# Optimization experiments

Measured on AMD Instinct MI355X. Metric: run time of the kernel, lower is better.

## Reference

```python
import jax, jax.numpy as jnp
import numpy as np

B, N, D, H, O = 20000, 32, 128, 256, 128
ATT_SLOPE = 0.01   # nn.LeakyReLU() default inside self.att
ALPHA = 0.2        # leakyrelu slope for attention scores


def _lrelu(v, slope):
    return jnp.where(v > 0, v, slope * v)


def setup_inputs() -> dict:
    key = jax.random.key(0)
    ks = jax.random.split(key, 6)
    x = jax.random.normal(ks[0], (B, D), dtype=jnp.float32)
    neibs = jax.random.normal(ks[1], (B * N, D), dtype=jnp.float32)
    # torch Linear weight is [out,in]; we store transposed [in,out] for x @ W
    W_att = jax.random.normal(ks[2], (D, H), dtype=jnp.float32) / np.sqrt(D)
    W_fcx = jax.random.normal(ks[3], (D, O), dtype=jnp.float32) / np.sqrt(D)
    W_fcn = jax.random.normal(ks[4], (D, O), dtype=jnp.float32) / np.sqrt(D)
    a = jax.random.normal(ks[5], (2 * H, 1), dtype=jnp.float32) * (1.414 * np.sqrt(6.0 / (2 * H + 1)))
    return {"x": x, "neibs": neibs, "W_att": W_att, "W_fcx": W_fcx, "W_fcn": W_fcn, "a": a}


def reference(x, neibs, W_att, W_fcx, W_fcn, a):
    b = x.shape[0]
    n = neibs.shape[0] // b
    # self.att = Linear(no bias) + LeakyReLU(default 0.01)
    x_att = _lrelu(x @ W_att, ATT_SLOPE)                       # [B,H]
    neib_att = _lrelu(neibs @ W_att, ATT_SLOPE).reshape(b, n, -1)  # [B,N,H]
    # cat([x_att.repeat, neib_att]) @ a  ==  x_att @ a[:H] + neib_att @ a[H:]
    h = W_att.shape[1]
    e = _lrelu(x_att @ a[:h, 0] + neib_att @ a[h:, 0][..., None] if False else
               (x_att @ a[:h, 0])[:, None] + jnp.einsum('bnh,h->bn', neib_att, a[h:, 0]), ALPHA)  # [B,N]
    attention = jax.nn.softmax(e, axis=1)                      # softmax over neighbors
    # dropout skipped (eval mode / training=False)
    agg_neib = jnp.einsum('bnd,bn->bd', neibs.reshape(b, n, -1), attention)  # [B,D]
    out = jnp.concatenate([x @ W_fcx, agg_neib @ W_fcn], axis=1)  # combine_fn = cat dim=1
    out = jax.nn.relu(out)                                     # activation
    return out
```

## Files before the change

### kernel.cpp

```cpp
#include <hip/hip_runtime.h>
#include <hip/hip_bf16.h>


#define BB 20000
#define NN 32
#define DD 128
#define HH 256
#define OO 128
#define MB 4
#define ROWS 144
#define AG0 132

typedef __bf16 bf16x8 __attribute__((ext_vector_type(8)));
typedef __bf16 bf16x4 __attribute__((ext_vector_type(4)));
typedef float f32x4 __attribute__((ext_vector_type(4)));

__global__ void prep_weights(const float* __restrict__ Watt,
                             const float* __restrict__ Wfcx,
                             const float* __restrict__ Wfcn,
                             __bf16* __restrict__ WaT,
                             __bf16* __restrict__ WcT) {
    int idx = blockIdx.x * 256 + threadIdx.x;
    int half = idx >> 15;
    int j = idx & 32767;
    int c = j >> 7, k = j & 127;
    if (half == 0) {
        WaT[j] = (__bf16)Watt[k * HH + c];
    } else {
        float wv = (c < OO) ? Wfcx[k * OO + c] : Wfcn[k * OO + (c - OO)];
        WcT[j] = (__bf16)wv;
    }
}

__launch_bounds__(256, 4)
__global__ void gat_fused(const float* __restrict__ x,
                          const float* __restrict__ neibs,
                          const float* __restrict__ a,
                          const __bf16* __restrict__ WaT,
                          const __bf16* __restrict__ WcT,
                          float* __restrict__ out) {
    __shared__ __bf16 rowsS[ROWS * 128];
    __shared__ float e_part[4][ROWS];
    __shared__ float att_s[MB][NN];

    const int tid = threadIdx.x;
    const int w   = tid >> 6;
    const int l   = tid & 63;
    const int lr  = l & 15;
    const int lg  = l >> 4;
    const int b0  = blockIdx.x * MB;
    char* rbase = (char*)rowsS;

    const int stbase = (tid >> 5) * 256 + ((8 * (tid & 31)) ^ ((tid >> 5) << 4));
    int abase[4];
#pragma unroll
    for (int ks = 0; ks < 4; ++ks)
        abase[ks] = lr * 256 + ((ks * 64 + lg * 16) ^ ((lr & 7) << 4));

    {
        const float4* np4 = (const float4*)(neibs + (size_t)b0 * NN * DD);
#pragma unroll
        for (int it = 0; it < 16; ++it) {
            float4 v = np4[it * 256 + tid];
            bf16x4 s = { (__bf16)v.x, (__bf16)v.y, (__bf16)v.z, (__bf16)v.w };
            *(bf16x4*)(rbase + stbase + it * 2048) = s;
        }
        if (tid < 128) {
            float4 v = ((const float4*)(x + (size_t)b0 * DD))[tid];
            bf16x4 s = { (__bf16)v.x, (__bf16)v.y, (__bf16)v.z, (__bf16)v.w };
            *(bf16x4*)(rbase + stbase + 32768) = s;
        }
    }

    bf16x8 bw[4][4];
    float cN[4][4];
#pragma unroll
    for (int c4 = 0; c4 < 4; ++c4) {
        int col = (w * 4 + c4) * 16 + lr;
#pragma unroll
        for (int ks = 0; ks < 4; ++ks)
            bw[c4][ks] = *(const bf16x8*)(WaT + col * 128 + ks * 32 + lg * 8);
#pragma unroll
        for (int i = 0; i < 4; ++i)
            cN[c4][i] = a[HH + (w * 4 + c4) * 16 + 4 * lg + i];
    }

    __syncthreads();

#pragma unroll
    for (int rt = 0; rt < 8; ++rt) {
        bf16x8 af[4];
#pragma unroll
        for (int ks = 0; ks < 4; ++ks)
            af[ks] = *(const bf16x8*)(rbase + abase[ks] + rt * 4096);
        f32x4 acc[4];
#pragma unroll
        for (int c4 = 0; c4 < 4; ++c4) acc[c4] = (f32x4){0.f, 0.f, 0.f, 0.f};
#pragma unroll
        for (int ks = 0; ks < 4; ++ks)
#pragma unroll
            for (int c4 = 0; c4 < 4; ++c4)
                acc[c4] = __builtin_amdgcn_mfma_f32_16x16x32_bf16(bw[c4][ks], af[ks], acc[c4], 0, 0, 0);
        float ep = 0.f;
#pragma unroll
        for (int c4 = 0; c4 < 4; ++c4)
#pragma unroll
            for (int i = 0; i < 4; ++i) {
                float v = acc[c4][i];
                ep = fmaf(cN[c4][i], fmaxf(v, 0.01f * v), ep);
            }
        ep += __shfl_xor(ep, 16);
        ep += __shfl_xor(ep, 32);
        if (l < 16) e_part[w][rt * 16 + l] = ep;
    }
    {
#pragma unroll
        for (int c4 = 0; c4 < 4; ++c4)
#pragma unroll
            for (int i = 0; i < 4; ++i)
                cN[c4][i] = a[(w * 4 + c4) * 16 + 4 * lg + i];
        bf16x8 af[4];
#pragma unroll
        for (int ks = 0; ks < 4; ++ks)
            af[ks] = *(const bf16x8*)(rbase + abase[ks] + 32768);
        f32x4 acc[4];
#pragma unroll
        for (int c4 = 0; c4 < 4; ++c4) acc[c4] = (f32x4){0.f, 0.f, 0.f, 0.f};
#pragma unroll
        for (int ks = 0; ks < 4; ++ks)
#pragma unroll
            for (int c4 = 0; c4 < 4; ++c4)
                acc[c4] = __builtin_amdgcn_mfma_f32_16x16x32_bf16(bw[c4][ks], af[ks], acc[c4], 0, 0, 0);
        float ep = 0.f;
#pragma unroll
        for (int c4 = 0; c4 < 4; ++c4)
#pragma unroll
            for (int i = 0; i < 4; ++i) {
                float v = acc[c4][i];
                ep = fmaf(cN[c4][i], fmaxf(v, 0.01f * v), ep);
            }
        ep += __shfl_xor(ep, 16);
        ep += __shfl_xor(ep, 32);
        if (l < 16) e_part[w][128 + l] = ep;
    }
    __syncthreads();

    if (tid < 128) {
        const int bloc = tid >> 5;
        const int nloc = tid & 31;
        float sn = e_part[0][tid] + e_part[1][tid] + e_part[2][tid] + e_part[3][tid];
        float sx = e_part[0][128 + bloc] + e_part[1][128 + bloc] +
                   e_part[2][128 + bloc] + e_part[3][128 + bloc];
        float e = sx + sn;
        e = (e > 0.f) ? e : 0.2f * e;
        float mx = e;
#pragma unroll
        for (int m = 16; m >= 1; m >>= 1) mx = fmaxf(mx, __shfl_xor(mx, m, 32));
        float ex = __expf(e - mx);
        float sum = ex;
#pragma unroll
        for (int m = 16; m >= 1; m >>= 1) sum += __shfl_xor(sum, m, 32);
        att_s[bloc][nloc] = ex / sum;
    }
    __syncthreads();

    bf16x8 bff[4][4];
#pragma unroll
    for (int c4 = 0; c4 < 4; ++c4)
#pragma unroll
        for (int ks = 0; ks < 4; ++ks)
            bff[c4][ks] = *(const bf16x8*)(WcT + ((w * 4 + c4) * 16 + lr) * 128 + ks * 32 + lg * 8);

    {
        const int half = l >> 5, li = l & 31;
        const int agbase = w * 8192 + 256 * half + ((8 * li) ^ (half << 4));
        float ag[4] = {0.f, 0.f, 0.f, 0.f};
#pragma unroll
        for (int i = 0; i < 16; ++i) {
            float wv = att_s[w][2 * i + half];
            bf16x4 v = *(const bf16x4*)(rbase + (agbase ^ ((2 * i & 7) << 4)) + 512 * i);
#pragma unroll
            for (int j = 0; j < 4; ++j) ag[j] = fmaf(wv, (float)v[j], ag[j]);
        }
#pragma unroll
        for (int j = 0; j < 4; ++j) ag[j] += __shfl_xor(ag[j], 32);
        if (half == 0) {
            int row = AG0 + w;
            int off = row * 256 + ((8 * li) ^ ((row & 7) << 4));
            bf16x4 s = { (__bf16)ag[0], (__bf16)ag[1], (__bf16)ag[2], (__bf16)ag[3] };
            *(bf16x4*)(rbase + off) = s;
        }
    }
    __syncthreads();

    {
        bf16x8 af[4];
#pragma unroll
        for (int ks = 0; ks < 4; ++ks)
            af[ks] = *(const bf16x8*)(rbase + abase[ks] + 32768);
        f32x4 acc[4];
#pragma unroll
        for (int c4 = 0; c4 < 4; ++c4) acc[c4] = (f32x4){0.f, 0.f, 0.f, 0.f};
#pragma unroll
        for (int ks = 0; ks < 4; ++ks)
#pragma unroll
            for (int c4 = 0; c4 < 4; ++c4)
                acc[c4] = __builtin_amdgcn_mfma_f32_16x16x32_bf16(af[ks], bff[c4][ks], acc[c4], 0, 0, 0);
#pragma unroll
        for (int c4 = 0; c4 < 4; ++c4) {
            int col = (w * 4 + c4) * 16 + lr;
#pragma unroll
            for (int reg = 0; reg < 4; ++reg) {
                int i = lg * 4 + reg;
                bool doit = (col < 128) ? (i < 4) : (i >= 4 && i < 8);
                if (doit) {
                    float v = fmaxf(acc[c4][reg], 0.f);
                    out[(size_t)(b0 + (i & 3)) * 256 + col] = v;
                }
            }
        }
    }
}

extern "C" void kernel_launch(void* const* d_in, const int* in_sizes, int n_in,
                              void* d_out, int out_size, void* d_ws, size_t ws_size,
                              hipStream_t stream) {
    const float* x    = (const float*)d_in[0];
    const float* nb   = (const float*)d_in[1];
    const float* Watt = (const float*)d_in[2];
    const float* Wfcx = (const float*)d_in[3];
    const float* Wfcn = (const float*)d_in[4];
    const float* a    = (const float*)d_in[5];
    __bf16* WaT = (__bf16*)d_ws;
    __bf16* WcT = WaT + 32768;
    float* o = (float*)d_out;

    prep_weights<<<256, 256, 0, stream>>>(Watt, Wfcx, Wfcn, WaT, WcT);
    gat_fused<<<BB / MB, 256, 0, stream>>>(x, nb, a, WaT, WcT, o);
}
```

Measured before the change: 126.6 us.

## Load MFMA operands directly from global memory instead of staging rows in LDS

Removes the 36KB LDS staging buffer for neighbor and x rows. Each wave now loads fp32 operands straight from global memory and converts them to bf16 in registers for the attention MFMAs. The softmax result stays in registers and is broadcast by shuffle, so the att_s array and one barrier go away. The aggregation re-reads neighbor rows from global memory (likely L2 hits) in fp32 instead of bf16 from LDS. The much smaller LDS footprint should allow higher occupancy, at the cost of more global and L2 traffic with less coalesced per-lane access.

```diff
diff --git a/kernel.cpp b/kernel.cpp
--- a/kernel.cpp
+++ b/kernel.cpp
@@ -8,12 +8,15 @@
 #define HH 256
 #define OO 128
 #define MB 4
-#define ROWS 144
-#define AG0 132
 
 typedef __bf16 bf16x8 __attribute__((ext_vector_type(8)));
-typedef __bf16 bf16x4 __attribute__((ext_vector_type(4)));
+typedef __bf16 bf16x2 __attribute__((ext_vector_type(2)));
 typedef float f32x4 __attribute__((ext_vector_type(4)));
+
+__device__ __forceinline__ bf16x8 cvt8(float4 u, float4 v) {
+    return (bf16x8){ (__bf16)u.x, (__bf16)u.y, (__bf16)u.z, (__bf16)u.w,
+                     (__bf16)v.x, (__bf16)v.y, (__bf16)v.z, (__bf16)v.w };
+}
 
 __global__ void prep_weights(const float* __restrict__ Watt,
                              const float* __restrict__ Wfcx,
@@ -39,9 +42,8 @@
                           const __bf16* __restrict__ WaT,
                           const __bf16* __restrict__ WcT,
                           float* __restrict__ out) {
-    __shared__ __bf16 rowsS[ROWS * 128];
-    __shared__ float e_part[4][ROWS];
-    __shared__ float att_s[MB][NN];
+    __shared__ float e_part[4][144];
+    __shared__ __bf16 aggL[4 * 136];
 
     const int tid = threadIdx.x;
     const int w   = tid >> 6;
@@ -49,28 +51,7 @@
     const int lr  = l & 15;
     const int lg  = l >> 4;
     const int b0  = blockIdx.x * MB;
-    char* rbase = (char*)rowsS;
-
-    const int stbase = (tid >> 5) * 256 + ((8 * (tid & 31)) ^ ((tid >> 5) << 4));
-    int abase[4];
-#pragma unroll
-    for (int ks = 0; ks < 4; ++ks)
-        abase[ks] = lr * 256 + ((ks * 64 + lg * 16) ^ ((lr & 7) << 4));
-
-    {
-        const float4* np4 = (const float4*)(neibs + (size_t)b0 * NN * DD);
-#pragma unroll
-        for (int it = 0; it < 16; ++it) {
-            float4 v = np4[it * 256 + tid];
-            bf16x4 s = { (__bf16)v.x, (__bf16)v.y, (__bf16)v.z, (__bf16)v.w };
-            *(bf16x4*)(rbase + stbase + it * 2048) = s;
-        }
-        if (tid < 128) {
-            float4 v = ((const float4*)(x + (size_t)b0 * DD))[tid];
-            bf16x4 s = { (__bf16)v.x, (__bf16)v.y, (__bf16)v.z, (__bf16)v.w };
-            *(bf16x4*)(rbase + stbase + 32768) = s;
-        }
-    }
+    const float* nb = neibs + (size_t)b0 * NN * DD;
 
     bf16x8 bw[4][4];
     float cN[4][4];
@@ -85,14 +66,14 @@
             cN[c4][i] = a[HH + (w * 4 + c4) * 16 + 4 * lg + i];
     }
 
-    __syncthreads();
-
 #pragma unroll
     for (int rt = 0; rt < 8; ++rt) {
         bf16x8 af[4];
 #pragma unroll
-        for (int ks = 0; ks < 4; ++ks)
-            af[ks] = *(const bf16x8*)(rbase + abase[ks] + rt * 4096);
+        for (int ks = 0; ks < 4; ++ks) {
+            const float* p = nb + (rt * 16 + lr) * 128 + ks * 32 + lg * 8;
+            af[ks] = cvt8(*(const float4*)p, *(const float4*)(p + 4));
+        }
         f32x4 acc[4];
 #pragma unroll
         for (int c4 = 0; c4 < 4; ++c4) acc[c4] = (f32x4){0.f, 0.f, 0.f, 0.f};
@@ -119,10 +100,13 @@
 #pragma unroll
             for (int i = 0; i < 4; ++i)
                 cN[c4][i] = a[(w * 4 + c4) * 16 + 4 * lg + i];
+        const float* xp = x + (size_t)(b0 + (lr & 3)) * 128;
         bf16x8 af[4];
 #pragma unroll
-        for (int ks = 0; ks < 4; ++ks)
-            af[ks] = *(const bf16x8*)(rbase + abase[ks] + 32768);
+        for (int ks = 0; ks < 4; ++ks) {
+            const float* p = xp + ks * 32 + lg * 8;
+            af[ks] = cvt8(*(const float4*)p, *(const float4*)(p + 4));
+        }
         f32x4 acc[4];
 #pragma unroll
         for (int c4 = 0; c4 < 4; ++c4) acc[c4] = (f32x4){0.f, 0.f, 0.f, 0.f};
@@ -145,13 +129,13 @@
     }
     __syncthreads();
 
-    if (tid < 128) {
-        const int bloc = tid >> 5;
-        const int nloc = tid & 31;
-        float sn = e_part[0][tid] + e_part[1][tid] + e_part[2][tid] + e_part[3][tid];
-        float sx = e_part[0][128 + bloc] + e_part[1][128 + bloc] +
-                   e_part[2][128 + bloc] + e_part[3][128 + bloc];
-        float e = sx + sn;
+    float att;
+    {
+        const int nl = l & 31;
+        const int idx = w * 32 + nl;
+        const int xr = 128 + w;
+        float e = e_part[0][idx] + e_part[1][idx] + e_part[2][idx] + e_part[3][idx]
+                + e_part[0][xr]  + e_part[1][xr]  + e_part[2][xr]  + e_part[3][xr];
         e = (e > 0.f) ? e : 0.2f * e;
         float mx = e;
 #pragma unroll
@@ -160,44 +144,46 @@
         float sum = ex;
 #pragma unroll
         for (int m = 16; m >= 1; m >>= 1) sum += __shfl_xor(sum, m, 32);
-        att_s[bloc][nloc] = ex / sum;
+        att = ex / sum;
+    }
+
+    bf16x8 bff[4][4];
+#pragma unroll
+    for (int c4 = 0; c4 < 4; ++c4)
+#pragma unroll
+        for (int ks = 0; ks < 4; ++ks)
+            bff[c4][ks] = *(const bf16x8*)(WcT + ((w * 4 + c4) * 16 + lr) * 128 + ks * 32 + lg * 8);
+
+    {
+        const float* rp = nb + (w * 32) * 128 + 2 * l;
+        float ag0 = 0.f, ag1 = 0.f;
+#pragma unroll 8
+        for (int n = 0; n < 32; ++n) {
+            float wv = __shfl(att, n);
+            float2 v = *(const float2*)(rp + n * 128);
+            ag0 = fmaf(wv, v.x, ag0);
+            ag1 = fmaf(wv, v.y, ag1);
+        }
+        bf16x2 s = { (__bf16)ag0, (__bf16)ag1 };
+        *(bf16x2*)((char*)aggL + w * 272 + 4 * l) = s;
     }
     __syncthreads();
 
-    bf16x8 bff[4][4];
-#pragma unroll
-    for (int c4 = 0; c4 < 4; ++c4)
-#pragma unroll
-        for (int ks = 0; ks < 4; ++ks)
-            bff[c4][ks] = *(const bf16x8*)(WcT + ((w * 4 + c4) * 16 + lr) * 128 + ks * 32 + lg * 8);
-
-    {
-        const int half = l >> 5, li = l & 31;
-        const int agbase = w * 8192 + 256 * half + ((8 * li) ^ (half << 4));
-        float ag[4] = {0.f, 0.f, 0.f, 0.f};
-#pragma unroll
-        for (int i = 0; i < 16; ++i) {
-            float wv = att_s[w][2 * i + half];
-            bf16x4 v = *(const bf16x4*)(rbase + (agbase ^ ((2 * i & 7) << 4)) + 512 * i);
-#pragma unroll
-            for (int j = 0; j < 4; ++j) ag[j] = fmaf(wv, (float)v[j], ag[j]);
-        }
-#pragma unroll
-        for (int j = 0; j < 4; ++j) ag[j] += __shfl_xor(ag[j], 32);
-        if (half == 0) {
-            int row = AG0 + w;
-            int off = row * 256 + ((8 * li) ^ ((row & 7) << 4));
-            bf16x4 s = { (__bf16)ag[0], (__bf16)ag[1], (__bf16)ag[2], (__bf16)ag[3] };
-            *(bf16x4*)(rbase + off) = s;
-        }
-    }
-    __syncthreads();
-
     {
         bf16x8 af[4];
-#pragma unroll
-        for (int ks = 0; ks < 4; ++ks)
-            af[ks] = *(const bf16x8*)(rbase + abase[ks] + 32768);
+        if (lr < 4) {
+            const float* xp = x + (size_t)(b0 + lr) * 128;
+#pragma unroll
+            for (int ks = 0; ks < 4; ++ks) {
+                const float* p = xp + ks * 32 + lg * 8;
+                af[ks] = cvt8(*(const float4*)p, *(const float4*)(p + 4));
+            }
+        } else {
+            const char* ap = (const char*)aggL + ((lr - 4) & 3) * 272;
+#pragma unroll
+            for (int ks = 0; ks < 4; ++ks)
+                af[ks] = *(const bf16x8*)(ap + ks * 64 + lg * 16);
+        }
         f32x4 acc[4];
 #pragma unroll
         for (int c4 = 0; c4 < 4; ++c4) acc[c4] = (f32x4){0.f, 0.f, 0.f, 0.f};
```

Result: slower. 274.3 us (+116.6%).

## Process two node groups per block, prefetching second group's neighbors during first

Applied to the files above, without the earlier changes.

Each block now handles two groups of 4 nodes (8 nodes total) with half the grid. The second group's neighbor rows are loaded into registers while the first group's softmax and aggregation run, then written to shared memory. The x projection for both groups and the final output GEMM are batched into one 16-row tile, and the MFMA rows for the x tile are fully used instead of mostly wasted. The cost is higher register pressure from 16 float4 prefetch registers and fewer blocks for latency hiding.

```diff
diff --git a/kernel.cpp b/kernel.cpp
--- a/kernel.cpp
+++ b/kernel.cpp
@@ -8,12 +8,14 @@
 #define HH 256
 #define OO 128
 #define MB 4
-#define ROWS 144
-#define AG0 132
+#define GRID 2500
 
 typedef __bf16 bf16x8 __attribute__((ext_vector_type(8)));
 typedef __bf16 bf16x4 __attribute__((ext_vector_type(4)));
 typedef float f32x4 __attribute__((ext_vector_type(4)));
+
+#define LBAR() do { asm volatile("s_waitcnt lgkmcnt(0)" ::: "memory"); \
+                    __builtin_amdgcn_s_barrier(); } while (0)
 
 __global__ void prep_weights(const float* __restrict__ Watt,
                              const float* __restrict__ Wfcx,
@@ -39,17 +41,20 @@
                           const __bf16* __restrict__ WaT,
                           const __bf16* __restrict__ WcT,
                           float* __restrict__ out) {
-    __shared__ __bf16 rowsS[ROWS * 128];
-    __shared__ float e_part[4][ROWS];
-    __shared__ float att_s[MB][NN];
+    __shared__ __bf16 rowsS[128 * 128];
+    __shared__ __bf16 xagg[16 * 128];
+    __shared__ float e_part[4][144];
+    __shared__ float att_s[4][32];
 
     const int tid = threadIdx.x;
     const int w   = tid >> 6;
     const int l   = tid & 63;
     const int lr  = l & 15;
     const int lg  = l >> 4;
-    const int b0  = blockIdx.x * MB;
-    char* rbase = (char*)rowsS;
+    const int g0  = (int)blockIdx.x * 2;
+    const int b0  = g0 * MB;
+    char* rb = (char*)rowsS;
+    char* xb = (char*)xagg;
 
     const int stbase = (tid >> 5) * 256 + ((8 * (tid & 31)) ^ ((tid >> 5) << 4));
     int abase[4];
@@ -58,18 +63,19 @@
         abase[ks] = lr * 256 + ((ks * 64 + lg * 16) ^ ((lr & 7) << 4));
 
     {
-        const float4* np4 = (const float4*)(neibs + (size_t)b0 * NN * DD);
+        const float4* np4 = (const float4*)neibs + (size_t)g0 * 4096;
 #pragma unroll
         for (int it = 0; it < 16; ++it) {
             float4 v = np4[it * 256 + tid];
             bf16x4 s = { (__bf16)v.x, (__bf16)v.y, (__bf16)v.z, (__bf16)v.w };
-            *(bf16x4*)(rbase + stbase + it * 2048) = s;
-        }
-        if (tid < 128) {
-            float4 v = ((const float4*)(x + (size_t)b0 * DD))[tid];
-            bf16x4 s = { (__bf16)v.x, (__bf16)v.y, (__bf16)v.z, (__bf16)v.w };
-            *(bf16x4*)(rbase + stbase + 32768) = s;
-        }
+            *(bf16x4*)(rb + stbase + it * 2048) = s;
+        }
+        float4 v = ((const float4*)x + (size_t)b0 * 32)[tid];
+        int r = tid >> 5;
+        int xrow = r + ((r >> 2) << 2);
+        unsigned off = xrow * 256 + ((8 * (tid & 31)) ^ ((xrow & 7) << 4));
+        bf16x4 s = { (__bf16)v.x, (__bf16)v.y, (__bf16)v.z, (__bf16)v.w };
+        *(bf16x4*)(xb + off) = s;
     }
 
     bf16x8 bw[4][4];
@@ -85,14 +91,90 @@
             cN[c4][i] = a[HH + (w * 4 + c4) * 16 + 4 * lg + i];
     }
 
-    __syncthreads();
-
-#pragma unroll
-    for (int rt = 0; rt < 8; ++rt) {
+    auto SCORE_NEIB = [&]() {
+#pragma unroll
+        for (int rt = 0; rt < 8; ++rt) {
+            bf16x8 af[4];
+#pragma unroll
+            for (int ks = 0; ks < 4; ++ks)
+                af[ks] = *(const bf16x8*)(rb + abase[ks] + rt * 4096);
+            f32x4 acc[4];
+#pragma unroll
+            for (int c4 = 0; c4 < 4; ++c4) acc[c4] = (f32x4){0.f, 0.f, 0.f, 0.f};
+#pragma unroll
+            for (int ks = 0; ks < 4; ++ks)
+#pragma unroll
+                for (int c4 = 0; c4 < 4; ++c4)
+                    acc[c4] = __builtin_amdgcn_mfma_f32_16x16x32_bf16(bw[c4][ks], af[ks], acc[c4], 0, 0, 0);
+            float ep = 0.f;
+#pragma unroll
+            for (int c4 = 0; c4 < 4; ++c4)
+#pragma unroll
+                for (int i = 0; i < 4; ++i) {
+                    float v = acc[c4][i];
+                    ep = fmaf(cN[c4][i], fmaxf(v, 0.01f * v), ep);
+                }
+            ep += __shfl_xor(ep, 16);
+            ep += __shfl_xor(ep, 32);
+            if (l < 16) e_part[w][rt * 16 + l] = ep;
+        }
+    };
+
+    auto SOFTMAX = [&](int xrbase) {
+        if (tid < 128) {
+            const int bloc = tid >> 5;
+            const int nloc = tid & 31;
+            float sn = e_part[0][tid] + e_part[1][tid] + e_part[2][tid] + e_part[3][tid];
+            int xr = xrbase + bloc;
+            float sx = e_part[0][xr] + e_part[1][xr] + e_part[2][xr] + e_part[3][xr];
+            float e = sx + sn;
+            e = (e > 0.f) ? e : 0.2f * e;
+            float mx = e;
+#pragma unroll
+            for (int m = 16; m >= 1; m >>= 1) mx = fmaxf(mx, __shfl_xor(mx, m, 32));
+            float ex = __expf(e - mx);
+            float sum = ex;
+#pragma unroll
+            for (int m = 16; m >= 1; m >>= 1) sum += __shfl_xor(sum, m, 32);
+            att_s[bloc][nloc] = ex / sum;
+        }
+    };
+
+    auto AGG = [&](int rowbase) {
+        const int half = l >> 5, li = l & 31;
+        const int agbase = w * 8192 + 256 * half + ((8 * li) ^ (half << 4));
+        float ag[4] = {0.f, 0.f, 0.f, 0.f};
+#pragma unroll
+        for (int i = 0; i < 16; ++i) {
+            float wv = att_s[w][2 * i + half];
+            bf16x4 v = *(const bf16x4*)(rb + (agbase ^ ((2 * i & 7) << 4)) + 512 * i);
+#pragma unroll
+            for (int j = 0; j < 4; ++j) ag[j] = fmaf(wv, (float)v[j], ag[j]);
+        }
+#pragma unroll
+        for (int j = 0; j < 4; ++j) ag[j] += __shfl_xor(ag[j], 32);
+        if (half == 0) {
+            int row = rowbase + w;
+            int off = row * 256 + ((8 * li) ^ ((row & 7) << 4));
+            bf16x4 s = { (__bf16)ag[0], (__bf16)ag[1], (__bf16)ag[2], (__bf16)ag[3] };
+            *(bf16x4*)(xb + off) = s;
+        }
+    };
+
+    __syncthreads();
+
+    SCORE_NEIB();
+    {
+        float cX[4][4];
+#pragma unroll
+        for (int c4 = 0; c4 < 4; ++c4)
+#pragma unroll
+            for (int i = 0; i < 4; ++i)
+                cX[c4][i] = a[(w * 4 + c4) * 16 + 4 * lg + i];
         bf16x8 af[4];
 #pragma unroll
         for (int ks = 0; ks < 4; ++ks)
-            af[ks] = *(const bf16x8*)(rbase + abase[ks] + rt * 4096);
+            af[ks] = *(const bf16x8*)(xb + abase[ks]);
         f32x4 acc[4];
 #pragma unroll
         for (int c4 = 0; c4 < 4; ++c4) acc[c4] = (f32x4){0.f, 0.f, 0.f, 0.f};
@@ -107,37 +189,7 @@
 #pragma unroll
             for (int i = 0; i < 4; ++i) {
                 float v = acc[c4][i];
-                ep = fmaf(cN[c4][i], fmaxf(v, 0.01f * v), ep);
-            }
-        ep += __shfl_xor(ep, 16);
-        ep += __shfl_xor(ep, 32);
-        if (l < 16) e_part[w][rt * 16 + l] = ep;
-    }
-    {
-#pragma unroll
-        for (int c4 = 0; c4 < 4; ++c4)
-#pragma unroll
-            for (int i = 0; i < 4; ++i)
-                cN[c4][i] = a[(w * 4 + c4) * 16 + 4 * lg + i];
-        bf16x8 af[4];
-#pragma unroll
-        for (int ks = 0; ks < 4; ++ks)
-            af[ks] = *(const bf16x8*)(rbase + abase[ks] + 32768);
-        f32x4 acc[4];
-#pragma unroll
-        for (int c4 = 0; c4 < 4; ++c4) acc[c4] = (f32x4){0.f, 0.f, 0.f, 0.f};
-#pragma unroll
-        for (int ks = 0; ks < 4; ++ks)
-#pragma unroll
-            for (int c4 = 0; c4 < 4; ++c4)
-                acc[c4] = __builtin_amdgcn_mfma_f32_16x16x32_bf16(bw[c4][ks], af[ks], acc[c4], 0, 0, 0);
-        float ep = 0.f;
-#pragma unroll
-        for (int c4 = 0; c4 < 4; ++c4)
-#pragma unroll
-            for (int i = 0; i < 4; ++i) {
-                float v = acc[c4][i];
-                ep = fmaf(cN[c4][i], fmaxf(v, 0.01f * v), ep);
+                ep = fmaf(cX[c4][i], fmaxf(v, 0.01f * v), ep);
             }
         ep += __shfl_xor(ep, 16);
         ep += __shfl_xor(ep, 32);
@@ -145,24 +197,30 @@
     }
     __syncthreads();
 
-    if (tid < 128) {
-        const int bloc = tid >> 5;
-        const int nloc = tid & 31;
-        float sn = e_part[0][tid] + e_part[1][tid] + e_part[2][tid] + e_part[3][tid];
-        float sx = e_part[0][128 + bloc] + e_part[1][128 + bloc] +
-                   e_part[2][128 + bloc] + e_part[3][128 + bloc];
-        float e = sx + sn;
-        e = (e > 0.f) ? e : 0.2f * e;
-        float mx = e;
-#pragma unroll
-        for (int m = 16; m >= 1; m >>= 1) mx = fmaxf(mx, __shfl_xor(mx, m, 32));
-        float ex = __expf(e - mx);
-        float sum = ex;
-#pragma unroll
-        for (int m = 16; m >= 1; m >>= 1) sum += __shfl_xor(sum, m, 32);
-        att_s[bloc][nloc] = ex / sum;
-    }
-    __syncthreads();
+    SOFTMAX(128);
+
+    float4 pf[16];
+    {
+        const float4* np1 = (const float4*)neibs + (size_t)(g0 + 1) * 4096;
+#pragma unroll
+        for (int it = 0; it < 16; ++it) pf[it] = np1[it * 256 + tid];
+    }
+
+    LBAR();
+    AGG(4);
+    LBAR();
+
+#pragma unroll
+    for (int it = 0; it < 16; ++it) {
+        bf16x4 s = { (__bf16)pf[it].x, (__bf16)pf[it].y, (__bf16)pf[it].z, (__bf16)pf[it].w };
+        *(bf16x4*)(rb + stbase + it * 2048) = s;
+    }
+    __syncthreads();
+
+    SCORE_NEIB();
+    __syncthreads();
+
+    SOFTMAX(136);
 
     bf16x8 bff[4][4];
 #pragma unroll
@@ -171,33 +229,15 @@
         for (int ks = 0; ks < 4; ++ks)
             bff[c4][ks] = *(const bf16x8*)(WcT + ((w * 4 + c4) * 16 + lr) * 128 + ks * 32 + lg * 8);
 
-    {
-        const int half = l >> 5, li = l & 31;
-        const int agbase = w * 8192 + 256 * half + ((8 * li) ^ (half << 4));
-        float ag[4] = {0.f, 0.f, 0.f, 0.f};
-#pragma unroll
-        for (int i = 0; i < 16; ++i) {
-            float wv = att_s[w][2 * i + half];
-            bf16x4 v = *(const bf16x4*)(rbase + (agbase ^ ((2 * i & 7) << 4)) + 512 * i);
-#pragma unroll
-            for (int j = 0; j < 4; ++j) ag[j] = fmaf(wv, (float)v[j], ag[j]);
-        }
-#pragma unroll
-        for (int j = 0; j < 4; ++j) ag[j] += __shfl_xor(ag[j], 32);
-        if (half == 0) {
-            int row = AG0 + w;
-            int off = row * 256 + ((8 * li) ^ ((row & 7) << 4));
-            bf16x4 s = { (__bf16)ag[0], (__bf16)ag[1], (__bf16)ag[2], (__bf16)ag[3] };
-            *(bf16x4*)(rbase + off) = s;
-        }
-    }
+    __syncthreads();
+    AGG(12);
     __syncthreads();
 
     {
         bf16x8 af[4];
 #pragma unroll
         for (int ks = 0; ks < 4; ++ks)
-            af[ks] = *(const bf16x8*)(rbase + abase[ks] + 32768);
+            af[ks] = *(const bf16x8*)(xb + abase[ks]);
         f32x4 acc[4];
 #pragma unroll
         for (int c4 = 0; c4 < 4; ++c4) acc[c4] = (f32x4){0.f, 0.f, 0.f, 0.f};
@@ -212,10 +252,10 @@
 #pragma unroll
             for (int reg = 0; reg < 4; ++reg) {
                 int i = lg * 4 + reg;
-                bool doit = (col < 128) ? (i < 4) : (i >= 4 && i < 8);
+                bool doit = ((col < 128) == ((i & 4) == 0));
                 if (doit) {
-                    float v = fmaxf(acc[c4][reg], 0.f);
-                    out[(size_t)(b0 + (i & 3)) * 256 + col] = v;
+                    int orow = b0 + (i & 3) + ((i >> 3) << 2);
+                    out[(size_t)orow * 256 + col] = fmaxf(acc[c4][reg], 0.f);
                 }
             }
         }
@@ -236,5 +276,5 @@
     float* o = (float*)d_out;
 
     prep_weights<<<256, 256, 0, stream>>>(Watt, Wfcx, Wfcn, WaT, WcT);
-    gat_fused<<<BB / MB, 256, 0, stream>>>(x, nb, a, WaT, WcT, o);
+    gat_fused<<<GRID, 256, 0, stream>>>(x, nb, a, WaT, WcT, o);
 }
```

Measured after the change: 258.8 us. 2.04x slower.
